# Optimization experiments

Measured on AMD Instinct MI355X. Metric: run time of the kernel, lower is better.

## Reference

```python
import jax, jax.numpy as jnp
import numpy as np

B, T, D, H = 4, 2048, 1024, 16
HD = D // H

def setup_inputs() -> dict:
    key = jax.random.key(0)
    ks = jax.random.split(key, 7)
    s = 1.0 / np.sqrt(D)
    return {
        "x": jax.random.normal(ks[0], (B, T, D), dtype=jnp.float32),
        "w_qkv": jax.random.uniform(ks[1], (D, 3 * D), jnp.float32, -s, s),
        "b_qkv": jax.random.uniform(ks[2], (3 * D,), jnp.float32, -s, s),
        "w_proj": jax.random.uniform(ks[3], (D, D), jnp.float32, -s, s),
        "b_proj": jax.random.uniform(ks[4], (D,), jnp.float32, -s, s),
        "ln_gamma": jnp.ones((D,), jnp.float32),
        "ln_beta": jnp.zeros((D,), jnp.float32),
    }

def reference(x, w_qkv, b_qkv, w_proj, b_proj, ln_gamma, ln_beta):
    eps = 1e-5
    scale = HD ** -0.5
    residual = x
    # Pre-norm LayerNorm over last dim
    mu = jnp.mean(x, axis=-1, keepdims=True)
    var = jnp.mean(jnp.square(x - mu), axis=-1, keepdims=True)
    xn = (x - mu) * jax.lax.rsqrt(var + eps) * ln_gamma + ln_beta
    # QKV projection: (B,T,3D) -> (3,B,H,T,HD)
    qkv = xn @ w_qkv + b_qkv
    qkv = qkv.reshape(B, T, 3, H, HD).transpose(2, 0, 3, 1, 4)
    q, k, v = qkv[0], qkv[1], qkv[2]
    # Scaled dot-product attention (full T x T scores, as in source)
    attn = jnp.einsum('bhqd,bhkd->bhqk', q, k) * scale
    attn = jax.nn.softmax(attn, axis=-1)
    out = jnp.einsum('bhqk,bhkd->bhqd', attn, v)
    out = out.transpose(0, 2, 1, 3).reshape(B, T, D)
    out = out @ w_proj + b_proj
    return residual + out
```

## Files before the change

kernel.cpp:

```cpp
#include <hip/hip_runtime.h>
#include <cstdint>
#include <cstddef>

#define B_ 4
#define T_ 2048
#define D_ 1024
#define H_ 16

typedef __attribute__((ext_vector_type(8))) short short8;
typedef __attribute__((ext_vector_type(4))) float f32x4;
typedef __attribute__((ext_vector_type(8))) unsigned short u16x8;

__device__ __forceinline__ unsigned short f2b16(float f) {
  union { float f; unsigned int u; } un; un.f = f;
  unsigned int r = un.u + 0x7fffu + ((un.u >> 16) & 1u);
  return (unsigned short)(r >> 16);
}
__device__ __forceinline__ void async_cp16(const void* g, void* l) {
  __builtin_amdgcn_global_load_lds((const __attribute__((address_space(1))) void*)g,
                                   (__attribute__((address_space(3))) void*)l,
                                   16, 0, 0);
}

__global__ __launch_bounds__(256) void ln_kernel(const float* __restrict__ x,
                                                 const float* __restrict__ gamma,
                                                 const float* __restrict__ beta,
                                                 unsigned short* __restrict__ xn) {
  const int row = blockIdx.x;
  const int t = threadIdx.x;
  const float4 v = ((const float4*)(x + (size_t)row * D_))[t];
  float s  = v.x + v.y + v.z + v.w;
  float s2 = v.x*v.x + v.y*v.y + v.z*v.z + v.w*v.w;
  #pragma unroll
  for (int off = 32; off > 0; off >>= 1) {
    s  += __shfl_down(s, off);
    s2 += __shfl_down(s2, off);
  }
  __shared__ float sh[8];
  const int wv = t >> 6, lane = t & 63;
  if (lane == 0) { sh[wv] = s; sh[4 + wv] = s2; }
  __syncthreads();
  if (t == 0) {
    float ts  = sh[0] + sh[1] + sh[2] + sh[3];
    float ts2 = sh[4] + sh[5] + sh[6] + sh[7];
    float mu  = ts * (1.0f / D_);
    float var = ts2 * (1.0f / D_) - mu * mu;
    sh[0] = mu;
    sh[1] = rsqrtf(var + 1e-5f);
  }
  __syncthreads();
  const float mu = sh[0], rs = sh[1];
  const float4 g  = ((const float4*)gamma)[t];
  const float4 bb = ((const float4*)beta)[t];
  ushort4 o;
  o.x = f2b16((v.x - mu) * rs * g.x + bb.x);
  o.y = f2b16((v.y - mu) * rs * g.y + bb.y);
  o.z = f2b16((v.z - mu) * rs * g.z + bb.z);
  o.w = f2b16((v.w - mu) * rs * g.w + bb.w);
  ((ushort4*)(xn + (size_t)row * D_))[t] = o;
}

__global__ __launch_bounds__(256) void transpose_cast(const float* __restrict__ w,
                                                      unsigned short* __restrict__ wT,
                                                      int K, int N) {
  __shared__ float tile[32][33];
  const int n0 = blockIdx.x * 32;
  const int k0 = blockIdx.y * 32;
  const int tx = threadIdx.x, ty = threadIdx.y;
  #pragma unroll
  for (int i = 0; i < 32; i += 8)
    tile[ty + i][tx] = w[(size_t)(k0 + ty + i) * N + n0 + tx];
  __syncthreads();
  #pragma unroll
  for (int i = 0; i < 32; i += 8)
    wT[(size_t)(n0 + ty + i) * K + k0 + tx] = f2b16(tile[tx][ty + i]);
}

__global__ __launch_bounds__(256) void transpose_v(const unsigned short* __restrict__ vB,
                                                   unsigned short* __restrict__ vtB) {
  __shared__ unsigned short tile[64 * 66];
  const int tid = threadIdx.x;
  const int bh = blockIdx.x;
  const int t0 = blockIdx.y * 64;
  const int lr = tid >> 2, lc = (tid & 3) * 16;
  const unsigned short* src = vB + ((size_t)bh * T_ + t0) * 64;
  *(u16x8*)&tile[lr * 66 + lc]     = *(const u16x8*)(src + (size_t)lr * 64 + lc);
  *(u16x8*)&tile[lr * 66 + lc + 8] = *(const u16x8*)(src + (size_t)lr * 64 + lc + 8);
  __syncthreads();
  const int dv = tid >> 2, cb = (tid & 3) * 16;
  unsigned short outv[16];
  #pragma unroll
  for (int j = 0; j < 16; ++j) {
    const int c = cb + j;
    const int t = (c & 32) | ((c & 4) << 2) | ((c & 16) >> 1) | ((c & 8) >> 1) | (c & 3);
    outv[j] = tile[t * 66 + dv];
  }
  unsigned short* dst = vtB + ((size_t)bh * 64 + dv) * T_ + t0 + cb;
  *(u16x8*)dst       = *(const u16x8*)&outv[0];
  *(u16x8*)(dst + 8) = *(const u16x8*)&outv[8];
}

__global__ __launch_bounds__(512, 2) void gemm256_qkv(const unsigned short* __restrict__ A,
                                                      const unsigned short* __restrict__ Bt,
                                                      const float* __restrict__ bias,
                                                      unsigned short* __restrict__ qB,
                                                      unsigned short* __restrict__ kB,
                                                      unsigned short* __restrict__ vB) {
  constexpr int K = 1024;
  constexpr int NT = K / 64;
  __shared__ __align__(16) unsigned short As[32768];
  __shared__ __align__(16) unsigned short Bs[32768];

  const int tid  = threadIdx.x;
  const int lane = tid & 63;
  const int wv   = tid >> 6;
  const int l15  = lane & 15, quad = lane >> 4;
  const int wr   = wv >> 1;
  const int wc   = wv & 1;

  const int w = (blockIdx.x & 7) * 48 + (blockIdx.x >> 3);
  const int tileM = (w & 31) * 256;
  const int tileN = (w >> 5) * 256;

  const int sr  = tid >> 3;
  const int scs = ((tid & 7) ^ (sr & 7)) * 8;
  const unsigned short* gA = A  + (size_t)(tileM + sr) * K + scs;
  const unsigned short* gB = Bt + (size_t)(tileN + sr) * K + scs;

  auto stageA = [&](int h, int ko, int wbuf) {
    const unsigned short* g = gA + (size_t)(h * 128) * K + ko;
    unsigned short* l = &As[wbuf * 16384 + h * 8192 + tid * 8];
    async_cp16(g, l);
    async_cp16(g + (size_t)64 * K, l + 4096);
  };
  auto stageB = [&](int h, int ko, int wbuf) {
    const unsigned short* g = gB + (size_t)(h * 128) * K + ko;
    unsigned short* l = &Bs[wbuf * 16384 + h * 8192 + tid * 8];
    async_cp16(g, l);
    async_cp16(g + (size_t)64 * K, l + 4096);
  };

  const int rA  = wr * 32 + l15;
  const int rB  = wc * 64 + l15;
  const int ck0 = ((0 + quad) ^ (l15 & 7)) * 8;
  const int ck1 = ((4 + quad) ^ (l15 & 7)) * 8;

  f32x4 acc[2][2][2][4] = {};

#define MFMA16(QM, QN, AF, BF)                                                          \
  do {                                                                                  \
    _Pragma("unroll") for (int fm = 0; fm < 2; ++fm)                                    \
    _Pragma("unroll") for (int fn = 0; fn < 4; ++fn) {                                  \
      acc[QM][QN][fm][fn] = __builtin_amdgcn_mfma_f32_16x16x32_bf16(                    \
          AF[fm][0], BF[fn][0], acc[QM][QN][fm][fn], 0, 0, 0);                          \
      acc[QM][QN][fm][fn] = __builtin_amdgcn_mfma_f32_16x16x32_bf16(                    \
          AF[fm][1], BF[fn][1], acc[QM][QN][fm][fn], 0, 0, 0);                          \
    }                                                                                   \
  } while (0)

  stageA(0, 0, 0);
  stageB(0, 0, 0);
  stageB(1, 0, 0);
  stageA(1, 0, 0);
  asm volatile("s_waitcnt vmcnt(4)" ::: "memory");
  asm volatile("s_barrier" ::: "memory");

  #pragma unroll 2
  for (int kt = 0; kt < NT; ++kt) {
    const int buf = kt & 1;
    const unsigned short* Ab = &As[buf * 16384];
    const unsigned short* Bb = &Bs[buf * 16384];
    const int wbuf = buf ^ 1;
    const bool st = (kt + 1) < NT;
    const int ko = (kt + 1) * 64;

    short8 a[2][2], b0[4][2], b1[4][2];

    #pragma unroll
    for (int fm = 0; fm < 2; ++fm) {
      a[fm][0] = *(const short8*)&Ab[(rA + fm * 16) * 64 + ck0];
      a[fm][1] = *(const short8*)&Ab[(rA + fm * 16) * 64 + ck1];
    }
    #pragma unroll
    for (int fn = 0; fn < 4; ++fn) {
      b0[fn][0] = *(const short8*)&Bb[(rB + fn * 16) * 64 + ck0];
      b0[fn][1] = *(const short8*)&Bb[(rB + fn * 16) * 64 + ck1];
    }
    if (st) stageA(0, ko, wbuf);
    asm volatile("s_waitcnt lgkmcnt(0)" ::: "memory");
    __builtin_amdgcn_sched_barrier(0);
    __builtin_amdgcn_s_setprio(1);
    MFMA16(0, 0, a, b0);
    __builtin_amdgcn_s_setprio(0);
    if (st) asm volatile("s_waitcnt vmcnt(4)" ::: "memory");
    else    asm volatile("s_waitcnt vmcnt(2)" ::: "memory");
    asm volatile("s_barrier" ::: "memory");

    #pragma unroll
    for (int fn = 0; fn < 4; ++fn) {
      b1[fn][0] = *(const short8*)&Bb[8192 + (rB + fn * 16) * 64 + ck0];
      b1[fn][1] = *(const short8*)&Bb[8192 + (rB + fn * 16) * 64 + ck1];
    }
    if (st) stageB(0, ko, wbuf);
    asm volatile("s_waitcnt lgkmcnt(0)" ::: "memory");
    __builtin_amdgcn_sched_barrier(0);
    __builtin_amdgcn_s_setprio(1);
    MFMA16(0, 1, a, b1);
    __builtin_amdgcn_s_setprio(0);
    if (st) asm volatile("s_waitcnt vmcnt(4)" ::: "memory");
    else    asm volatile("s_waitcnt vmcnt(0)" ::: "memory");
    asm volatile("s_barrier" ::: "memory");

    #pragma unroll
    for (int fm = 0; fm < 2; ++fm) {
      a[fm][0] = *(const short8*)&Ab[8192 + (rA + fm * 16) * 64 + ck0];
      a[fm][1] = *(const short8*)&Ab[8192 + (rA + fm * 16) * 64 + ck1];
    }
    if (st) stageB(1, ko, wbuf);
    asm volatile("s_waitcnt lgkmcnt(0)" ::: "memory");
    __builtin_amdgcn_sched_barrier(0);
    __builtin_amdgcn_s_setprio(1);
    MFMA16(1, 0, a, b0);
    __builtin_amdgcn_s_setprio(0);
    asm volatile("s_barrier" ::: "memory");

    if (st) stageA(1, ko, wbuf);
    __builtin_amdgcn_s_setprio(1);
    MFMA16(1, 1, a, b1);
    __builtin_amdgcn_s_setprio(0);
    if (st) asm volatile("s_waitcnt vmcnt(4)" ::: "memory");
    asm volatile("s_barrier" ::: "memory");
  }
#undef MFMA16

  unsigned short* E = &As[wv * 2304];
  #pragma unroll
  for (int qm = 0; qm < 2; ++qm) {
    #pragma unroll
    for (int qn = 0; qn < 2; ++qn) {
      const int colBase = tileN + qn * 128 + wc * 64;
      const int rowBase = tileM + qm * 128 + wr * 32;
      #pragma unroll
      for (int fn = 0; fn < 4; ++fn) {
        const int col = colBase + fn * 16 + l15;
        const float bv = bias[col];
        const float sc = (col < 1024) ? 0.180336880f : 1.0f;
        #pragma unroll
        for (int fm = 0; fm < 2; ++fm)
          #pragma unroll
          for (int r = 0; r < 4; ++r)
            E[(fm * 16 + quad * 4 + r) * 72 + fn * 16 + l15] =
                f2b16((acc[qm][qn][fm][fn][r] + bv) * sc);
      }
      const int secq = colBase >> 10;
      const int hh   = (colBase & 1023) >> 6;
      unsigned short* outSec = (secq == 0) ? qB : (secq == 1) ? kB : vB;
      #pragma unroll
      for (int it = 0; it < 4; ++it) {
        const int lrow = it * 8 + (lane >> 3);
        const int row = rowBase + lrow;
        const int b_ = row >> 11, t = row & 2047;
        const u16x8 val = *(const u16x8*)&E[lrow * 72 + (lane & 7) * 8];
        *(u16x8*)(outSec + ((size_t)(b_ * 16 + hh) * T_ + t) * 64 + (lane & 7) * 8) = val;
      }
    }
  }
}

template <int MODE>
__global__ __launch_bounds__(256) void gemm_bt(const unsigned short* __restrict__ A,
                                               const unsigned short* __restrict__ Bt,
                                               const float* __restrict__ bias,
                                               const float* __restrict__ resid,
                                               float* __restrict__ outF,
                                               int M, int N, int K) {
  __shared__ unsigned short As[128 * 32];
  __shared__ unsigned short Bs[128 * 32];
  const int tid  = threadIdx.x;
  const int lane = tid & 63;
  const int wv   = tid >> 6;
  const int wm   = (wv & 1) * 64;
  const int wn   = (wv >> 1) * 64;
  const int tileM = blockIdx.x * 128;
  const int tileN = blockIdx.y * 128;
  const int l15 = lane & 15, quad = lane >> 4;
  const int sRow = tid >> 2;
  const int sCol = (tid & 3) * 8;

  f32x4 acc[4][4] = {};

  const unsigned short* aG0 = A  + (size_t)(tileM + sRow) * K + sCol;
  const unsigned short* aG1 = A  + (size_t)(tileM + 64 + sRow) * K + sCol;
  const unsigned short* bG0 = Bt + (size_t)(tileN + sRow) * K + sCol;
  const unsigned short* bG1 = Bt + (size_t)(tileN + 64 + sRow) * K + sCol;
  unsigned short* lA0 = &As[tid * 8];
  unsigned short* lA1 = &As[2048 + tid * 8];
  unsigned short* lB0 = &Bs[tid * 8];
  unsigned short* lB1 = &Bs[2048 + tid * 8];

  for (int k0 = 0; k0 < K; k0 += 32) {
    async_cp16(aG0 + k0, lA0);
    async_cp16(aG1 + k0, lA1);
    async_cp16(bG0 + k0, lB0);
    async_cp16(bG1 + k0, lB1);
    __syncthreads();

    short8 a[4], b[4];
    #pragma unroll
    for (int i = 0; i < 4; ++i) {
      a[i] = *(const short8*)&As[(wm + i * 16 + l15) * 32 + quad * 8];
      b[i] = *(const short8*)&Bs[(wn + i * 16 + l15) * 32 + quad * 8];
    }
    #pragma unroll
    for (int mi = 0; mi < 4; ++mi)
      #pragma unroll
      for (int ni = 0; ni < 4; ++ni)
        acc[mi][ni] = __builtin_amdgcn_mfma_f32_16x16x32_bf16(a[mi], b[ni], acc[mi][ni], 0, 0, 0);
    __syncthreads();
  }

  #pragma unroll
  for (int ni = 0; ni < 4; ++ni) {
    const int col = tileN + wn + ni * 16 + l15;
    const float bv = bias[col];
    #pragma unroll
    for (int mi = 0; mi < 4; ++mi) {
      #pragma unroll
      for (int r = 0; r < 4; ++r) {
        const int row = tileM + wm + mi * 16 + quad * 4 + r;
        const size_t idx = (size_t)row * N + col;
        outF[idx] = acc[mi][ni][r] + bv + resid[idx];
      }
    }
  }
}

__global__ __launch_bounds__(256, 4) void attn_mfma(const unsigned short* __restrict__ qB,
                                                    const unsigned short* __restrict__ kB,
                                                    const unsigned short* __restrict__ vtB,
                                                    unsigned short* __restrict__ aout) {
  __shared__ unsigned short Ks[2][64 * 64];
  __shared__ unsigned short Vs[2][64 * 64];

  const int tid = threadIdx.x;
  const int bid = blockIdx.x;
  const int bh = bid & 63;
  const int qb = bid >> 6;
  const int b = bh >> 4, h = bh & 15;
  const int wv = tid >> 6, lane = tid & 63;
  const int l15 = lane & 15, quad = lane >> 4;

  const unsigned short* qP = qB  + (size_t)bh * T_ * 64;
  const unsigned short* kP = kB  + (size_t)bh * T_ * 64;
  const unsigned short* vP = vtB + (size_t)bh * 64 * T_;
  const int q0 = qb * 128 + wv * 32;

  short8 qf[2][2];
  #pragma unroll
  for (int mi = 0; mi < 2; ++mi)
    #pragma unroll
    for (int ks = 0; ks < 2; ++ks)
      qf[mi][ks] = *(const short8*)(qP + ((size_t)(q0 + mi * 16 + l15)) * 64 + ks * 32 + quad * 8);

  const short8 onesf = {0x3F80, 0x3F80, 0x3F80, 0x3F80, 0x3F80, 0x3F80, 0x3F80, 0x3F80};
  f32x4 accO[2][5] = {};

  const int lrow  = lane >> 3;
  const int lchnk = (lane & 7) ^ (lrow & 7);
  const size_t kOff0 = (size_t)((wv * 2 + 0) * 8 + lrow) * 64 + lchnk * 8;
  const size_t kOff1 = (size_t)((wv * 2 + 1) * 8 + lrow) * 64 + lchnk * 8;
  const size_t vOff0 = (size_t)((wv * 2 + 0) * 8 + lrow) * T_ + lchnk * 8;
  const size_t vOff1 = (size_t)((wv * 2 + 1) * 8 + lrow) * T_ + lchnk * 8;
  const int lOff0 = (wv * 2 + 0) * 512 + lane * 8;
  const int lOff1 = (wv * 2 + 1) * 512 + lane * 8;

  async_cp16(kP + kOff0, &Ks[0][lOff0]);
  async_cp16(kP + kOff1, &Ks[0][lOff1]);
  async_cp16(vP + vOff0, &Vs[0][lOff0]);
  async_cp16(vP + vOff1, &Vs[0][lOff1]);
  __syncthreads();

  for (int kt = 0; kt < 32; ++kt) {
    const int buf = kt & 1;
    if (kt + 1 < 32) {
      const unsigned short* kg = kP + (size_t)(kt + 1) * 64 * 64;
      const unsigned short* vg = vP + (kt + 1) * 64;
      async_cp16(kg + kOff0, &Ks[buf ^ 1][lOff0]);
      async_cp16(kg + kOff1, &Ks[buf ^ 1][lOff1]);
      async_cp16(vg + vOff0, &Vs[buf ^ 1][lOff0]);
      async_cp16(vg + vOff1, &Vs[buf ^ 1][lOff1]);
    }
    const unsigned short* K_ = Ks[buf];
    const unsigned short* V_ = Vs[buf];

    f32x4 accT[4][2] = {};
    #pragma unroll
    for (int ks = 0; ks < 2; ++ks) {
      #pragma unroll
      for (int cc = 0; cc < 4; ++cc) {
        const short8 kb = *(const short8*)&K_[(cc * 16 + l15) * 64 +
                                              (((ks << 2) | quad) ^ (l15 & 7)) * 8];
        accT[cc][0] = __builtin_amdgcn_mfma_f32_16x16x32_bf16(kb, qf[0][ks], accT[cc][0], 0, 0, 0);
        accT[cc][1] = __builtin_amdgcn_mfma_f32_16x16x32_bf16(kb, qf[1][ks], accT[cc][1], 0, 0, 0);
      }
    }

    short8 pa[2][2];
    #pragma unroll
    for (int mi = 0; mi < 2; ++mi) {
      #pragma unroll
      for (int ks = 0; ks < 2; ++ks) {
        union { unsigned short u[8]; short8 s; } pk;
        #pragma unroll
        for (int r = 0; r < 4; ++r) {
          union { float f; unsigned int u; } e0, e1;
          e0.f = __builtin_amdgcn_exp2f(accT[2 * ks + 0][mi][r]);
          e1.f = __builtin_amdgcn_exp2f(accT[2 * ks + 1][mi][r]);
          pk.u[r]     = (unsigned short)(e0.u >> 16);
          pk.u[4 + r] = (unsigned short)(e1.u >> 16);
        }
        pa[mi][ks] = pk.s;
      }
    }

    #pragma unroll
    for (int ks = 0; ks < 2; ++ks) {
      short8 vb[4];
      #pragma unroll
      for (int nj = 0; nj < 4; ++nj)
        vb[nj] = *(const short8*)&V_[(nj * 16 + l15) * 64 +
                                     (((ks << 2) | quad) ^ (l15 & 7)) * 8];
      #pragma unroll
      for (int mi = 0; mi < 2; ++mi) {
        #pragma unroll
        for (int nj = 0; nj < 4; ++nj)
          accO[mi][nj] = __builtin_amdgcn_mfma_f32_16x16x32_bf16(pa[mi][ks], vb[nj], accO[mi][nj], 0, 0, 0);
        accO[mi][4] = __builtin_amdgcn_mfma_f32_16x16x32_bf16(pa[mi][ks], onesf, accO[mi][4], 0, 0, 0);
      }
    }

    __syncthreads();
  }

  #pragma unroll
  for (int mi = 0; mi < 2; ++mi) {
    #pragma unroll
    for (int r = 0; r < 4; ++r) {
      const float inv = 1.0f / accO[mi][4][r];
      const int row = q0 + mi * 16 + quad * 4 + r;
      unsigned short* op = aout + (size_t)(b * T_ + row) * D_ + h * 64 + l15;
      #pragma unroll
      for (int nj = 0; nj < 4; ++nj)
        op[nj * 16] = f2b16(accO[mi][nj][r] * inv);
    }
  }
}

extern "C" void kernel_launch(void* const* d_in, const int* in_sizes, int n_in,
                              void* d_out, int out_size, void* d_ws, size_t ws_size,
                              hipStream_t stream) {
  const float* x      = (const float*)d_in[0];
  const float* w_qkv  = (const float*)d_in[1];
  const float* b_qkv  = (const float*)d_in[2];
  const float* w_proj = (const float*)d_in[3];
  const float* b_proj = (const float*)d_in[4];
  const float* ln_g   = (const float*)d_in[5];
  const float* ln_b   = (const float*)d_in[6];
  float* out = (float*)d_out;

  char* ws = (char*)d_ws;
  unsigned short* xn   = (unsigned short*)(ws);
  unsigned short* wTq  = (unsigned short*)(ws + (size_t)(16 << 20));
  unsigned short* wTp  = (unsigned short*)(ws + (size_t)(22 << 20));
  unsigned short* qBuf = (unsigned short*)(ws + (size_t)(24 << 20));
  unsigned short* kBuf = (unsigned short*)(ws + (size_t)(40 << 20));
  unsigned short* vBuf = (unsigned short*)(ws + (size_t)(56 << 20));
  unsigned short* vtB  = (unsigned short*)(ws + (size_t)(72 << 20));
  unsigned short* aout = xn;

  ln_kernel<<<8192, 256, 0, stream>>>(x, ln_g, ln_b, xn);
  transpose_cast<<<dim3(96, 32), dim3(32, 8), 0, stream>>>(w_qkv, wTq, 1024, 3072);
  transpose_cast<<<dim3(32, 32), dim3(32, 8), 0, stream>>>(w_proj, wTp, 1024, 1024);
  gemm256_qkv<<<384, 512, 0, stream>>>(xn, wTq, b_qkv, qBuf, kBuf, vBuf);
  transpose_v<<<dim3(64, 32), 256, 0, stream>>>(vBuf, vtB);
  attn_mfma<<<1024, 256, 0, stream>>>(qBuf, kBuf, vtB, aout);
  gemm_bt<1><<<dim3(64, 8), 256, 0, stream>>>(aout, wTp, b_proj, x, out, 8192, 1024, 1024);
}
```

Measured before the change: 281.7 us.

## Use templated 128x256 pipelined GEMM for both QKV and output projections

The 256x256 QKV GEMM kernel becomes a templated 128x256-tile kernel. It is launched with 768 blocks for QKV and also replaces the simple 128x128 single-buffered output-projection GEMM, which had no prefetch, with the 8-phase double-buffered async pipeline and a fused bias+residual epilogue. Smaller M tiles cut LDS use and give more blocks to fill CUs. In exchange, the QKV GEMM gets less reuse of each B tile and the vmcnt wait counts have to be retuned.

```diff
diff --git a/kernel.cpp b/kernel.cpp
--- a/kernel.cpp
+++ b/kernel.cpp
@@ -20,6 +20,9 @@
   __builtin_amdgcn_global_load_lds((const __attribute__((address_space(1))) void*)g,
                                    (__attribute__((address_space(3))) void*)l,
                                    16, 0, 0);
+}
+__device__ __forceinline__ f32x4 mfma16(short8 a, short8 b, f32x4 c) {
+  return __builtin_amdgcn_mfma_f32_16x16x32_bf16(a, b, c, 0, 0, 0);
 }
 
 __global__ __launch_bounds__(256) void ln_kernel(const float* __restrict__ x,
@@ -100,15 +103,18 @@
   *(u16x8*)(dst + 8) = *(const u16x8*)&outv[8];
 }
 
-__global__ __launch_bounds__(512, 2) void gemm256_qkv(const unsigned short* __restrict__ A,
-                                                      const unsigned short* __restrict__ Bt,
-                                                      const float* __restrict__ bias,
-                                                      unsigned short* __restrict__ qB,
-                                                      unsigned short* __restrict__ kB,
-                                                      unsigned short* __restrict__ vB) {
+template <int MODE, int NN>
+__global__ __launch_bounds__(512, 2) void gemm8p(const unsigned short* __restrict__ A,
+                                                 const unsigned short* __restrict__ Bt,
+                                                 const float* __restrict__ bias,
+                                                 const float* __restrict__ resid,
+                                                 unsigned short* __restrict__ qB,
+                                                 unsigned short* __restrict__ kB,
+                                                 unsigned short* __restrict__ vB,
+                                                 float* __restrict__ outF) {
   constexpr int K = 1024;
-  constexpr int NT = K / 64;
-  __shared__ __align__(16) unsigned short As[32768];
+  constexpr int NT = 16;
+  __shared__ __align__(16) unsigned short As[16384];
   __shared__ __align__(16) unsigned short Bs[32768];
 
   const int tid  = threadIdx.x;
@@ -118,82 +124,67 @@
   const int wr   = wv >> 1;
   const int wc   = wv & 1;
 
-  const int w = (blockIdx.x & 7) * 48 + (blockIdx.x >> 3);
-  const int tileM = (w & 31) * 256;
-  const int tileN = (w >> 5) * 256;
+  constexpr int CPX = (64 * (NN / 256)) / 8;
+  const int w = (blockIdx.x & 7) * CPX + (blockIdx.x >> 3);
+  const int tileM = (w & 63) * 128;
+  const int tileN = (w >> 6) * 256;
 
   const int sr  = tid >> 3;
   const int scs = ((tid & 7) ^ (sr & 7)) * 8;
   const unsigned short* gA = A  + (size_t)(tileM + sr) * K + scs;
   const unsigned short* gB = Bt + (size_t)(tileN + sr) * K + scs;
 
-  auto stageA = [&](int h, int ko, int wbuf) {
-    const unsigned short* g = gA + (size_t)(h * 128) * K + ko;
-    unsigned short* l = &As[wbuf * 16384 + h * 8192 + tid * 8];
+  auto stA = [&](int h, int ko, int wb) {
+    async_cp16(gA + (size_t)(h * 64) * K + ko, &As[wb * 8192 + h * 4096 + tid * 8]);
+  };
+  auto stB = [&](int h, int ko, int wb) {
+    const unsigned short* g = gB + (size_t)(h * 128) * K + ko;
+    unsigned short* l = &Bs[wb * 16384 + h * 8192 + tid * 8];
     async_cp16(g, l);
     async_cp16(g + (size_t)64 * K, l + 4096);
   };
-  auto stageB = [&](int h, int ko, int wbuf) {
-    const unsigned short* g = gB + (size_t)(h * 128) * K + ko;
-    unsigned short* l = &Bs[wbuf * 16384 + h * 8192 + tid * 8];
-    async_cp16(g, l);
-    async_cp16(g + (size_t)64 * K, l + 4096);
-  };
-
-  const int rA  = wr * 32 + l15;
+
+  const int rA  = wr * 16 + l15;
   const int rB  = wc * 64 + l15;
   const int ck0 = ((0 + quad) ^ (l15 & 7)) * 8;
   const int ck1 = ((4 + quad) ^ (l15 & 7)) * 8;
 
-  f32x4 acc[2][2][2][4] = {};
-
-#define MFMA16(QM, QN, AF, BF)                                                          \
-  do {                                                                                  \
-    _Pragma("unroll") for (int fm = 0; fm < 2; ++fm)                                    \
-    _Pragma("unroll") for (int fn = 0; fn < 4; ++fn) {                                  \
-      acc[QM][QN][fm][fn] = __builtin_amdgcn_mfma_f32_16x16x32_bf16(                    \
-          AF[fm][0], BF[fn][0], acc[QM][QN][fm][fn], 0, 0, 0);                          \
-      acc[QM][QN][fm][fn] = __builtin_amdgcn_mfma_f32_16x16x32_bf16(                    \
-          AF[fm][1], BF[fn][1], acc[QM][QN][fm][fn], 0, 0, 0);                          \
-    }                                                                                   \
-  } while (0)
-
-  stageA(0, 0, 0);
-  stageB(0, 0, 0);
-  stageB(1, 0, 0);
-  stageA(1, 0, 0);
-  asm volatile("s_waitcnt vmcnt(4)" ::: "memory");
+  f32x4 acc[2][2][4] = {};
+
+  stA(0, 0, 0); stB(0, 0, 0); stB(1, 0, 0); stA(1, 0, 0);
+  asm volatile("s_waitcnt vmcnt(3)" ::: "memory");
   asm volatile("s_barrier" ::: "memory");
 
   #pragma unroll 2
   for (int kt = 0; kt < NT; ++kt) {
     const int buf = kt & 1;
-    const unsigned short* Ab = &As[buf * 16384];
+    const unsigned short* Ab = &As[buf * 8192];
     const unsigned short* Bb = &Bs[buf * 16384];
-    const int wbuf = buf ^ 1;
+    const int wb = buf ^ 1;
     const bool st = (kt + 1) < NT;
     const int ko = (kt + 1) * 64;
 
-    short8 a[2][2], b0[4][2], b1[4][2];
-
-    #pragma unroll
-    for (int fm = 0; fm < 2; ++fm) {
-      a[fm][0] = *(const short8*)&Ab[(rA + fm * 16) * 64 + ck0];
-      a[fm][1] = *(const short8*)&Ab[(rA + fm * 16) * 64 + ck1];
-    }
+    short8 a[2], b0[4][2], b1[4][2];
+
+    a[0] = *(const short8*)&Ab[rA * 64 + ck0];
+    a[1] = *(const short8*)&Ab[rA * 64 + ck1];
     #pragma unroll
     for (int fn = 0; fn < 4; ++fn) {
       b0[fn][0] = *(const short8*)&Bb[(rB + fn * 16) * 64 + ck0];
       b0[fn][1] = *(const short8*)&Bb[(rB + fn * 16) * 64 + ck1];
     }
-    if (st) stageA(0, ko, wbuf);
+    if (st) stA(0, ko, wb);
     asm volatile("s_waitcnt lgkmcnt(0)" ::: "memory");
     __builtin_amdgcn_sched_barrier(0);
     __builtin_amdgcn_s_setprio(1);
-    MFMA16(0, 0, a, b0);
+    #pragma unroll
+    for (int fn = 0; fn < 4; ++fn) {
+      acc[0][0][fn] = mfma16(a[0], b0[fn][0], acc[0][0][fn]);
+      acc[0][0][fn] = mfma16(a[1], b0[fn][1], acc[0][0][fn]);
+    }
     __builtin_amdgcn_s_setprio(0);
-    if (st) asm volatile("s_waitcnt vmcnt(4)" ::: "memory");
-    else    asm volatile("s_waitcnt vmcnt(2)" ::: "memory");
+    if (st) asm volatile("s_waitcnt vmcnt(2)" ::: "memory");
+    else    asm volatile("s_waitcnt vmcnt(1)" ::: "memory");
     asm volatile("s_barrier" ::: "memory");
 
     #pragma unroll
@@ -201,135 +192,93 @@
       b1[fn][0] = *(const short8*)&Bb[8192 + (rB + fn * 16) * 64 + ck0];
       b1[fn][1] = *(const short8*)&Bb[8192 + (rB + fn * 16) * 64 + ck1];
     }
-    if (st) stageB(0, ko, wbuf);
+    if (st) stB(0, ko, wb);
     asm volatile("s_waitcnt lgkmcnt(0)" ::: "memory");
     __builtin_amdgcn_sched_barrier(0);
     __builtin_amdgcn_s_setprio(1);
-    MFMA16(0, 1, a, b1);
+    #pragma unroll
+    for (int fn = 0; fn < 4; ++fn) {
+      acc[0][1][fn] = mfma16(a[0], b1[fn][0], acc[0][1][fn]);
+      acc[0][1][fn] = mfma16(a[1], b1[fn][1], acc[0][1][fn]);
+    }
     __builtin_amdgcn_s_setprio(0);
-    if (st) asm volatile("s_waitcnt vmcnt(4)" ::: "memory");
+    if (st) asm volatile("s_waitcnt vmcnt(3)" ::: "memory");
     else    asm volatile("s_waitcnt vmcnt(0)" ::: "memory");
     asm volatile("s_barrier" ::: "memory");
 
-    #pragma unroll
-    for (int fm = 0; fm < 2; ++fm) {
-      a[fm][0] = *(const short8*)&Ab[8192 + (rA + fm * 16) * 64 + ck0];
-      a[fm][1] = *(const short8*)&Ab[8192 + (rA + fm * 16) * 64 + ck1];
-    }
-    if (st) stageB(1, ko, wbuf);
+    a[0] = *(const short8*)&Ab[4096 + rA * 64 + ck0];
+    a[1] = *(const short8*)&Ab[4096 + rA * 64 + ck1];
+    if (st) stB(1, ko, wb);
     asm volatile("s_waitcnt lgkmcnt(0)" ::: "memory");
     __builtin_amdgcn_sched_barrier(0);
     __builtin_amdgcn_s_setprio(1);
-    MFMA16(1, 0, a, b0);
+    #pragma unroll
+    for (int fn = 0; fn < 4; ++fn) {
+      acc[1][0][fn] = mfma16(a[0], b0[fn][0], acc[1][0][fn]);
+      acc[1][0][fn] = mfma16(a[1], b0[fn][1], acc[1][0][fn]);
+    }
     __builtin_amdgcn_s_setprio(0);
     asm volatile("s_barrier" ::: "memory");
 
-    if (st) stageA(1, ko, wbuf);
+    if (st) stA(1, ko, wb);
     __builtin_amdgcn_s_setprio(1);
-    MFMA16(1, 1, a, b1);
+    #pragma unroll
+    for (int fn = 0; fn < 4; ++fn) {
+      acc[1][1][fn] = mfma16(a[0], b1[fn][0], acc[1][1][fn]);
+      acc[1][1][fn] = mfma16(a[1], b1[fn][1], acc[1][1][fn]);
+    }
     __builtin_amdgcn_s_setprio(0);
-    if (st) asm volatile("s_waitcnt vmcnt(4)" ::: "memory");
+    if (st) asm volatile("s_waitcnt vmcnt(3)" ::: "memory");
     asm volatile("s_barrier" ::: "memory");
   }
-#undef MFMA16
-
-  unsigned short* E = &As[wv * 2304];
-  #pragma unroll
-  for (int qm = 0; qm < 2; ++qm) {
-    #pragma unroll
-    for (int qn = 0; qn < 2; ++qn) {
-      const int colBase = tileN + qn * 128 + wc * 64;
-      const int rowBase = tileM + qm * 128 + wr * 32;
-      #pragma unroll
-      for (int fn = 0; fn < 4; ++fn) {
-        const int col = colBase + fn * 16 + l15;
-        const float bv = bias[col];
-        const float sc = (col < 1024) ? 0.180336880f : 1.0f;
+
+  if constexpr (MODE == 0) {
+    unsigned short* E = &As[wv * 1152];
+    #pragma unroll
+    for (int qm = 0; qm < 2; ++qm) {
+      #pragma unroll
+      for (int qn = 0; qn < 2; ++qn) {
+        const int colBase = tileN + qn * 128 + wc * 64;
+        const int rowBase = tileM + qm * 64 + wr * 16;
         #pragma unroll
-        for (int fm = 0; fm < 2; ++fm)
+        for (int fn = 0; fn < 4; ++fn) {
+          const int col = colBase + fn * 16 + l15;
+          const float bv = bias[col];
+          const float sc = (col < 1024) ? 0.180336880f : 1.0f;
           #pragma unroll
           for (int r = 0; r < 4; ++r)
-            E[(fm * 16 + quad * 4 + r) * 72 + fn * 16 + l15] =
-                f2b16((acc[qm][qn][fm][fn][r] + bv) * sc);
+            E[(quad * 4 + r) * 72 + fn * 16 + l15] =
+                f2b16((acc[qm][qn][fn][r] + bv) * sc);
+        }
+        const int secq = colBase >> 10;
+        const int hh   = (colBase & 1023) >> 6;
+        unsigned short* outSec = (secq == 0) ? qB : (secq == 1) ? kB : vB;
+        #pragma unroll
+        for (int it = 0; it < 2; ++it) {
+          const int lrow = it * 8 + (lane >> 3);
+          const int row = rowBase + lrow;
+          const int b_ = row >> 11, t = row & 2047;
+          const u16x8 val = *(const u16x8*)&E[lrow * 72 + (lane & 7) * 8];
+          *(u16x8*)(outSec + ((size_t)(b_ * 16 + hh) * T_ + t) * 64 + (lane & 7) * 8) = val;
+        }
       }
-      const int secq = colBase >> 10;
-      const int hh   = (colBase & 1023) >> 6;
-      unsigned short* outSec = (secq == 0) ? qB : (secq == 1) ? kB : vB;
-      #pragma unroll
-      for (int it = 0; it < 4; ++it) {
-        const int lrow = it * 8 + (lane >> 3);
-        const int row = rowBase + lrow;
-        const int b_ = row >> 11, t = row & 2047;
-        const u16x8 val = *(const u16x8*)&E[lrow * 72 + (lane & 7) * 8];
-        *(u16x8*)(outSec + ((size_t)(b_ * 16 + hh) * T_ + t) * 64 + (lane & 7) * 8) = val;
-      }
-    }
-  }
-}
-
-template <int MODE>
-__global__ __launch_bounds__(256) void gemm_bt(const unsigned short* __restrict__ A,
-                                               const unsigned short* __restrict__ Bt,
-                                               const float* __restrict__ bias,
-                                               const float* __restrict__ resid,
-                                               float* __restrict__ outF,
-                                               int M, int N, int K) {
-  __shared__ unsigned short As[128 * 32];
-  __shared__ unsigned short Bs[128 * 32];
-  const int tid  = threadIdx.x;
-  const int lane = tid & 63;
-  const int wv   = tid >> 6;
-  const int wm   = (wv & 1) * 64;
-  const int wn   = (wv >> 1) * 64;
-  const int tileM = blockIdx.x * 128;
-  const int tileN = blockIdx.y * 128;
-  const int l15 = lane & 15, quad = lane >> 4;
-  const int sRow = tid >> 2;
-  const int sCol = (tid & 3) * 8;
-
-  f32x4 acc[4][4] = {};
-
-  const unsigned short* aG0 = A  + (size_t)(tileM + sRow) * K + sCol;
-  const unsigned short* aG1 = A  + (size_t)(tileM + 64 + sRow) * K + sCol;
-  const unsigned short* bG0 = Bt + (size_t)(tileN + sRow) * K + sCol;
-  const unsigned short* bG1 = Bt + (size_t)(tileN + 64 + sRow) * K + sCol;
-  unsigned short* lA0 = &As[tid * 8];
-  unsigned short* lA1 = &As[2048 + tid * 8];
-  unsigned short* lB0 = &Bs[tid * 8];
-  unsigned short* lB1 = &Bs[2048 + tid * 8];
-
-  for (int k0 = 0; k0 < K; k0 += 32) {
-    async_cp16(aG0 + k0, lA0);
-    async_cp16(aG1 + k0, lA1);
-    async_cp16(bG0 + k0, lB0);
-    async_cp16(bG1 + k0, lB1);
-    __syncthreads();
-
-    short8 a[4], b[4];
-    #pragma unroll
-    for (int i = 0; i < 4; ++i) {
-      a[i] = *(const short8*)&As[(wm + i * 16 + l15) * 32 + quad * 8];
-      b[i] = *(const short8*)&Bs[(wn + i * 16 + l15) * 32 + quad * 8];
-    }
-    #pragma unroll
-    for (int mi = 0; mi < 4; ++mi)
-      #pragma unroll
-      for (int ni = 0; ni < 4; ++ni)
-        acc[mi][ni] = __builtin_amdgcn_mfma_f32_16x16x32_bf16(a[mi], b[ni], acc[mi][ni], 0, 0, 0);
-    __syncthreads();
-  }
-
-  #pragma unroll
-  for (int ni = 0; ni < 4; ++ni) {
-    const int col = tileN + wn + ni * 16 + l15;
-    const float bv = bias[col];
-    #pragma unroll
-    for (int mi = 0; mi < 4; ++mi) {
-      #pragma unroll
-      for (int r = 0; r < 4; ++r) {
-        const int row = tileM + wm + mi * 16 + quad * 4 + r;
-        const size_t idx = (size_t)row * N + col;
-        outF[idx] = acc[mi][ni][r] + bv + resid[idx];
+    }
+  } else {
+    #pragma unroll
+    for (int qm = 0; qm < 2; ++qm) {
+      #pragma unroll
+      for (int qn = 0; qn < 2; ++qn) {
+        #pragma unroll
+        for (int fn = 0; fn < 4; ++fn) {
+          const int col = tileN + qn * 128 + wc * 64 + fn * 16 + l15;
+          const float bv = bias[col];
+          #pragma unroll
+          for (int r = 0; r < 4; ++r) {
+            const int row = tileM + qm * 64 + wr * 16 + quad * 4 + r;
+            const size_t idx = (size_t)row * NN + col;
+            outF[idx] = acc[qm][qn][fn][r] + bv + resid[idx];
+          }
+        }
       }
     }
   }
@@ -400,8 +349,8 @@
       for (int cc = 0; cc < 4; ++cc) {
         const short8 kb = *(const short8*)&K_[(cc * 16 + l15) * 64 +
                                               (((ks << 2) | quad) ^ (l15 & 7)) * 8];
-        accT[cc][0] = __builtin_amdgcn_mfma_f32_16x16x32_bf16(kb, qf[0][ks], accT[cc][0], 0, 0, 0);
-        accT[cc][1] = __builtin_amdgcn_mfma_f32_16x16x32_bf16(kb, qf[1][ks], accT[cc][1], 0, 0, 0);
+        accT[cc][0] = mfma16(kb, qf[0][ks], accT[cc][0]);
+        accT[cc][1] = mfma16(kb, qf[1][ks], accT[cc][1]);
       }
     }
 
@@ -434,8 +383,8 @@
       for (int mi = 0; mi < 2; ++mi) {
         #pragma unroll
         for (int nj = 0; nj < 4; ++nj)
-          accO[mi][nj] = __builtin_amdgcn_mfma_f32_16x16x32_bf16(pa[mi][ks], vb[nj], accO[mi][nj], 0, 0, 0);
-        accO[mi][4] = __builtin_amdgcn_mfma_f32_16x16x32_bf16(pa[mi][ks], onesf, accO[mi][4], 0, 0, 0);
+          accO[mi][nj] = mfma16(pa[mi][ks], vb[nj], accO[mi][nj]);
+        accO[mi][4] = mfma16(pa[mi][ks], onesf, accO[mi][4]);
       }
     }
 
@@ -481,8 +430,10 @@
   ln_kernel<<<8192, 256, 0, stream>>>(x, ln_g, ln_b, xn);
   transpose_cast<<<dim3(96, 32), dim3(32, 8), 0, stream>>>(w_qkv, wTq, 1024, 3072);
   transpose_cast<<<dim3(32, 32), dim3(32, 8), 0, stream>>>(w_proj, wTp, 1024, 1024);
-  gemm256_qkv<<<384, 512, 0, stream>>>(xn, wTq, b_qkv, qBuf, kBuf, vBuf);
+  gemm8p<0, 3072><<<768, 512, 0, stream>>>(xn, wTq, b_qkv, nullptr,
+                                           qBuf, kBuf, vBuf, nullptr);
   transpose_v<<<dim3(64, 32), 256, 0, stream>>>(vBuf, vtB);
   attn_mfma<<<1024, 256, 0, stream>>>(qBuf, kBuf, vtB, aout);
-  gemm_bt<1><<<dim3(64, 8), 256, 0, stream>>>(aout, wTp, b_proj, x, out, 8192, 1024, 1024);
-}
+  gemm8p<1, 1024><<<256, 512, 0, stream>>>(aout, wTp, b_proj, x,
+                                           nullptr, nullptr, nullptr, out);
+}
```

Measured after the change: 270.2 us. 4.1% less time.
